# Optimization experiments

Measured on AMD Instinct MI355X. Metric: run time of the kernel, lower is better.

## Reference

```python
import jax, jax.numpy as jnp
import numpy as np

B, T, H, IN = 1024, 512, 128, 1


def setup_inputs() -> dict:
    key = jax.random.key(0)
    ks = jax.random.split(key, 12)
    s = 1.0 / np.sqrt(H)  # torch LSTMCell/Linear uniform init scale
    u = lambda k, shape: jax.random.uniform(k, shape, jnp.float32, -s, s)
    return {
        "x": jax.random.normal(ks[0], (B, T, IN), jnp.float32),
        "Wih1": u(ks[1], (4 * H, IN)),
        "Whh1": u(ks[2], (4 * H, H)),
        "bih1": u(ks[3], (4 * H,)),
        "bhh1": u(ks[4], (4 * H,)),
        "Wih2": u(ks[5], (4 * H, H)),
        "Whh2": u(ks[6], (4 * H, H)),
        "bih2": u(ks[7], (4 * H,)),
        "bhh2": u(ks[8], (4 * H,)),
        "Wl": u(ks[9], (1, H)),
        "bl": u(ks[10], (1,)),
    }


def _lstm_cell(x, h, c, Wih, Whh, bih, bhh):
    # gates: [B, 4H], torch gate order: i, f, g, o
    gates = x @ Wih.T + h @ Whh.T + (bih + bhh)
    i, f, g, o = jnp.split(gates, 4, axis=-1)
    i = jax.nn.sigmoid(i)
    f = jax.nn.sigmoid(f)
    g = jnp.tanh(g)
    o = jax.nn.sigmoid(o)
    c_new = f * c + i * g
    h_new = o * jnp.tanh(c_new)
    return h_new, c_new


def reference(x, Wih1, Whh1, bih1, bhh1, Wih2, Whh2, bih2, bhh2, Wl, bl):
    b, t, _ = x.shape
    h = Wih1.shape[0] // 4
    z = jnp.zeros((b, h), x.dtype)

    def step(carry, x_t):
        h1, c1, h2, c2 = carry
        h1, c1 = _lstm_cell(x_t, h1, c1, Wih1, Whh1, bih1, bhh1)
        h2, c2 = _lstm_cell(h1, h2, c2, Wih2, Whh2, bih2, bhh2)
        return (h1, c1, h2, c2), None

    xs = jnp.transpose(x, (1, 0, 2))  # [T, B, IN]
    (h1, c1, h2, c2), _ = jax.lax.scan(step, (z, z, z, z), xs)
    # module stacks per-step linear outputs then keeps [:, -1] -> last step only
    return h2 @ Wl.T + bl  # [B, 1]
```

## Files before the change

### kernel.cpp

```cpp
#include <hip/hip_runtime.h>
#include <hip/hip_fp16.h>

#define TT 512
#define RR 4

using f16   = _Float16;
using f16x8 = __attribute__((ext_vector_type(8))) _Float16;
using f32x4 = __attribute__((ext_vector_type(4))) float;

__device__ __forceinline__ float sigm(float x) {
    return __builtin_amdgcn_rcpf(1.0f + __builtin_amdgcn_exp2f(x * -1.44269504f));
}
__device__ __forceinline__ float tanh_(float x) {
    return 1.0f - 2.0f * __builtin_amdgcn_rcpf(1.0f + __builtin_amdgcn_exp2f(x * 2.88539008f));
}

__global__ __launch_bounds__(512, 2) void lstm2_fused(
    const float* __restrict__ x,
    const float* __restrict__ Wih1,
    const float* __restrict__ Whh1,
    const float* __restrict__ bih1,
    const float* __restrict__ bhh1,
    const float* __restrict__ Wih2,
    const float* __restrict__ Whh2,
    const float* __restrict__ bih2,
    const float* __restrict__ bhh2,
    const float* __restrict__ Wl,
    const float* __restrict__ bl,
    float* __restrict__ out)
{
    __shared__ char smem[24576];

    const int tid  = threadIdx.x;
    const int w    = tid >> 6;
    const int lane = tid & 63;
    const int r    = lane & 15;
    const int q    = lane >> 4;
    const int rowbase = blockIdx.x * RR;

    {
        unsigned* hz = (unsigned*)smem;
        #pragma unroll
        for (int i = 0; i < 8; ++i) hz[tid + i * 512] = 0u;
    }

    float b1o[4], b2o[4], w1o[4];
    #pragma unroll
    for (int g = 0; g < 4; ++g) {
        int n = g * 128 + w * 16 + r;
        b1o[g] = bih1[n] + bhh1[n];
        b2o[g] = bih2[n] + bhh2[n];
        w1o[g] = Wih1[n];
    }
    const float wlv = Wl[w * 16 + r];
    const float bl0 = bl[0];

    f16x8 wr1[4][4], w2i[4][4], w2h[4][4];
    #pragma unroll
    for (int g = 0; g < 4; ++g) {
        int n = g * 128 + w * 16 + r;
        #pragma unroll
        for (int kt = 0; kt < 4; ++kt) {
            int k0 = kt * 32 + q * 8;
            const float4* p1 = (const float4*)(Whh1 + n * 128 + k0);
            const float4* pi = (const float4*)(Wih2 + n * 128 + k0);
            const float4* ph = (const float4*)(Whh2 + n * 128 + k0);
            float4 a1v = p1[0], b1v = p1[1];
            float4 ai = pi[0], bi = pi[1];
            float4 ah = ph[0], bh = ph[1];
            wr1[g][kt] = f16x8{ (f16)a1v.x,(f16)a1v.y,(f16)a1v.z,(f16)a1v.w,
                                (f16)b1v.x,(f16)b1v.y,(f16)b1v.z,(f16)b1v.w };
            w2i[g][kt] = f16x8{ (f16)ai.x,(f16)ai.y,(f16)ai.z,(f16)ai.w,
                                (f16)bi.x,(f16)bi.y,(f16)bi.z,(f16)bi.w };
            w2h[g][kt] = f16x8{ (f16)ah.x,(f16)ah.y,(f16)ah.z,(f16)ah.w,
                                (f16)bh.x,(f16)bh.y,(f16)bh.z,(f16)bh.w };
        }
    }

    int afrag[4];
    #pragma unroll
    for (int kt = 0; kt < 4; ++kt)
        afrag[kt] = r * 256 + ((kt * 64 + q * 16) ^ ((r & 7) << 4));
    const int hwoff = q * 256 + ((w * 32 + r * 2) ^ (q << 4));
    char* const gbase = smem + 16384 + w * 1024;

    float c1 = 0.f, c2 = 0.f, h2fin = 0.f;

    __syncthreads();

    char* const h1base = smem;
    char* const h2base = smem + 8192;

    for (int t = 0; t < TT; ++t) {
        const int p = t & 1;
        char* h1r = h1base + p * 4096;
        char* h1w = h1base + (p ^ 1) * 4096;
        char* h2r = h2base + p * 4096;
        char* h2w = h2base + (p ^ 1) * 4096;

        const float xv = x[(rowbase + q) * TT + t];

        f32x4 acc[4] = {{0.f,0.f,0.f,0.f},{0.f,0.f,0.f,0.f},
                        {0.f,0.f,0.f,0.f},{0.f,0.f,0.f,0.f}};
        #pragma unroll
        for (int kt = 0; kt < 4; ++kt) {
            f16x8 a1 = *(const f16x8*)(h1r + afrag[kt]);
            #pragma unroll
            for (int g = 0; g < 4; ++g)
                acc[g] = __builtin_amdgcn_mfma_f32_16x16x32_f16(a1, wr1[g][kt], acc[g], 0, 0, 0);
        }
        if (q == 0) {
            #pragma unroll
            for (int g = 0; g < 4; ++g)
                *(f32x4*)(gbase + g * 256 + r * 16) = acc[g];
        }
        {
            float pre[4];
            #pragma unroll
            for (int g = 0; g < 4; ++g)
                pre[g] = ((const float*)(gbase + g * 256 + r * 16))[q]
                         + fmaf(xv, w1o[g], b1o[g]);
            float gi = sigm (pre[0]);
            float gf = sigm (pre[1]);
            float gg = tanh_(pre[2]);
            float go = sigm (pre[3]);
            c1 = gf * c1 + gi * gg;
            float h1v = go * tanh_(c1);
            *(f16*)(h1w + hwoff) = (f16)h1v;
        }

        __syncthreads();

        f32x4 acc2[4] = {{0.f,0.f,0.f,0.f},{0.f,0.f,0.f,0.f},
                         {0.f,0.f,0.f,0.f},{0.f,0.f,0.f,0.f}};
        #pragma unroll
        for (int kt = 0; kt < 4; ++kt) {
            f16x8 ah1 = *(const f16x8*)(h1w + afrag[kt]);
            f16x8 ah2 = *(const f16x8*)(h2r + afrag[kt]);
            #pragma unroll
            for (int g = 0; g < 4; ++g)
                acc2[g] = __builtin_amdgcn_mfma_f32_16x16x32_f16(ah1, w2i[g][kt], acc2[g], 0, 0, 0);
            #pragma unroll
            for (int g = 0; g < 4; ++g)
                acc2[g] = __builtin_amdgcn_mfma_f32_16x16x32_f16(ah2, w2h[g][kt], acc2[g], 0, 0, 0);
        }
        if (q == 0) {
            #pragma unroll
            for (int g = 0; g < 4; ++g)
                *(f32x4*)(gbase + g * 256 + r * 16) = acc2[g];
        }
        {
            float pre[4];
            #pragma unroll
            for (int g = 0; g < 4; ++g)
                pre[g] = ((const float*)(gbase + g * 256 + r * 16))[q] + b2o[g];
            float gi = sigm (pre[0]);
            float gf = sigm (pre[1]);
            float gg = tanh_(pre[2]);
            float go = sigm (pre[3]);
            c2 = gf * c2 + gi * gg;
            float h2v = go * tanh_(c2);
            h2fin = h2v;
            *(f16*)(h2w + hwoff) = (f16)h2v;
        }

        __syncthreads();
    }

    float v = h2fin * wlv;
    v += __shfl_xor(v, 1);
    v += __shfl_xor(v, 2);
    v += __shfl_xor(v, 4);
    v += __shfl_xor(v, 8);
    float* red = (float*)(smem + 16384);
    if (r == 0) red[q * 8 + w] = v;
    __syncthreads();
    if (tid < RR) {
        float a = bl0;
        #pragma unroll
        for (int s = 0; s < 8; ++s) a += red[tid * 8 + s];
        out[rowbase + tid] = a;
    }
}

extern "C" void kernel_launch(void* const* d_in, const int* in_sizes, int n_in,
                              void* d_out, int out_size, void* d_ws, size_t ws_size,
                              hipStream_t stream) {
    const float* x    = (const float*)d_in[0];
    const float* Wih1 = (const float*)d_in[1];
    const float* Whh1 = (const float*)d_in[2];
    const float* bih1 = (const float*)d_in[3];
    const float* bhh1 = (const float*)d_in[4];
    const float* Wih2 = (const float*)d_in[5];
    const float* Whh2 = (const float*)d_in[6];
    const float* bih2 = (const float*)d_in[7];
    const float* bhh2 = (const float*)d_in[8];
    const float* Wl   = (const float*)d_in[9];
    const float* bl   = (const float*)d_in[10];
    float* out = (float*)d_out;

    lstm2_fused<<<dim3(256), dim3(512), 0, stream>>>(
        x, Wih1, Whh1, bih1, bhh1, Wih2, Whh2, bih2, bhh2, Wl, bl, out);
}
```

Measured before the change: 887.7 us.

## Specialize waves per LSTM layer and pipeline layer 2 one step behind

Splits the eight waves into four layer-1 waves and four layer-2 waves, with layer 2 lagging one timestep so each iteration needs a single barrier instead of two. Each wave now covers 32 hidden units, and the layer-2 recurrent weights are staged as fp16 in a large swizzled dynamic shared buffer. This is meant to cut per-step synchronization and let both layers run concurrently. In exchange, the layer-2 waves issue twice as many MFMAs, read B fragments from LDS, and the large shared allocation limits residency to one block per CU.

```diff
diff --git a/kernel.cpp b/kernel.cpp
--- a/kernel.cpp
+++ b/kernel.cpp
@@ -15,7 +15,7 @@
     return 1.0f - 2.0f * __builtin_amdgcn_rcpf(1.0f + __builtin_amdgcn_exp2f(x * 2.88539008f));
 }
 
-__global__ __launch_bounds__(512, 2) void lstm2_fused(
+__global__ __launch_bounds__(512, 2) void lstm2_spec(
     const float* __restrict__ x,
     const float* __restrict__ Wih1,
     const float* __restrict__ Whh1,
@@ -29,7 +29,11 @@
     const float* __restrict__ bl,
     float* __restrict__ out)
 {
-    __shared__ char smem[24576];
+    extern __shared__ char smem[];
+    char* const whh2L  = smem;
+    char* const h1m    = smem + 131072;
+    char* const h2m    = smem + 133120;
+    char* const strips = smem + 135168;
 
     const int tid  = threadIdx.x;
     const int w    = tid >> 6;
@@ -37,148 +41,182 @@
     const int r    = lane & 15;
     const int q    = lane >> 4;
     const int rowbase = blockIdx.x * RR;
+    const bool isL1 = (w < 4);
+    const int  jj   = isL1 ? w : (w - 4);
 
     {
-        unsigned* hz = (unsigned*)smem;
+        unsigned* z = (unsigned*)h1m;
+        z[tid] = 0u; z[tid + 512] = 0u;
+    }
+    for (int it = 0; it < 64; ++it) {
+        int pp = tid + it * 512;
+        int n  = pp >> 6;
+        int kp = pp & 63;
+        float2 v = *(const float2*)(Whh2 + n * 128 + kp * 2);
+        union { f16 h[2]; unsigned u; } cv;
+        cv.h[0] = (f16)v.x; cv.h[1] = (f16)v.y;
+        *(unsigned*)(whh2L + n * 256 + ((kp * 4) ^ ((n & 7) << 4))) = cv.u;
+    }
+
+    float bo[2][4], w1o[2][4];
+    #pragma unroll
+    for (int t2 = 0; t2 < 2; ++t2)
         #pragma unroll
-        for (int i = 0; i < 8; ++i) hz[tid + i * 512] = 0u;
-    }
-
-    float b1o[4], b2o[4], w1o[4];
-    #pragma unroll
-    for (int g = 0; g < 4; ++g) {
-        int n = g * 128 + w * 16 + r;
-        b1o[g] = bih1[n] + bhh1[n];
-        b2o[g] = bih2[n] + bhh2[n];
-        w1o[g] = Wih1[n];
-    }
-    const float wlv = Wl[w * 16 + r];
+        for (int g = 0; g < 4; ++g) {
+            int n = g * 128 + jj * 32 + t2 * 16 + r;
+            if (isL1) { bo[t2][g] = bih1[n] + bhh1[n]; w1o[t2][g] = Wih1[n]; }
+            else      { bo[t2][g] = bih2[n] + bhh2[n]; w1o[t2][g] = 0.f; }
+        }
+    float wl0 = 0.f, wl1 = 0.f;
+    if (!isL1) { wl0 = Wl[jj * 32 + r]; wl1 = Wl[jj * 32 + 16 + r]; }
     const float bl0 = bl[0];
 
-    f16x8 wr1[4][4], w2i[4][4], w2h[4][4];
-    #pragma unroll
-    for (int g = 0; g < 4; ++g) {
-        int n = g * 128 + w * 16 + r;
+    const float* const Wreg = isL1 ? Whh1 : Wih2;
+    f16x8 wreg[4][2][4];
+    #pragma unroll
+    for (int g = 0; g < 4; ++g)
         #pragma unroll
-        for (int kt = 0; kt < 4; ++kt) {
-            int k0 = kt * 32 + q * 8;
-            const float4* p1 = (const float4*)(Whh1 + n * 128 + k0);
-            const float4* pi = (const float4*)(Wih2 + n * 128 + k0);
-            const float4* ph = (const float4*)(Whh2 + n * 128 + k0);
-            float4 a1v = p1[0], b1v = p1[1];
-            float4 ai = pi[0], bi = pi[1];
-            float4 ah = ph[0], bh = ph[1];
-            wr1[g][kt] = f16x8{ (f16)a1v.x,(f16)a1v.y,(f16)a1v.z,(f16)a1v.w,
-                                (f16)b1v.x,(f16)b1v.y,(f16)b1v.z,(f16)b1v.w };
-            w2i[g][kt] = f16x8{ (f16)ai.x,(f16)ai.y,(f16)ai.z,(f16)ai.w,
-                                (f16)bi.x,(f16)bi.y,(f16)bi.z,(f16)bi.w };
-            w2h[g][kt] = f16x8{ (f16)ah.x,(f16)ah.y,(f16)ah.z,(f16)ah.w,
-                                (f16)bh.x,(f16)bh.y,(f16)bh.z,(f16)bh.w };
+        for (int t2 = 0; t2 < 2; ++t2) {
+            int n = g * 128 + jj * 32 + t2 * 16 + r;
+            #pragma unroll
+            for (int kt = 0; kt < 4; ++kt) {
+                const float4* p = (const float4*)(Wreg + n * 128 + kt * 32 + q * 8);
+                float4 a = p[0], b = p[1];
+                wreg[g][t2][kt] = f16x8{ (f16)a.x,(f16)a.y,(f16)a.z,(f16)a.w,
+                                         (f16)b.x,(f16)b.y,(f16)b.z,(f16)b.w };
+            }
         }
-    }
-
-    int afrag[4];
-    #pragma unroll
-    for (int kt = 0; kt < 4; ++kt)
-        afrag[kt] = r * 256 + ((kt * 64 + q * 16) ^ ((r & 7) << 4));
-    const int hwoff = q * 256 + ((w * 32 + r * 2) ^ (q << 4));
-    char* const gbase = smem + 16384 + w * 1024;
-
-    float c1 = 0.f, c2 = 0.f, h2fin = 0.f;
+
+    const int swz = (r & 7) << 4;
+    int kxo[4];
+    #pragma unroll
+    for (int kt = 0; kt < 4; ++kt) kxo[kt] = (kt * 64 + q * 16) ^ swz;
+    int afo[4];
+    #pragma unroll
+    for (int kt = 0; kt < 4; ++kt) afo[kt] = r * 256 + kxo[kt];
+    int nbt[2];
+    #pragma unroll
+    for (int t2 = 0; t2 < 2; ++t2) nbt[t2] = (jj * 32 + t2 * 16 + r) * 256;
+    int hwo[2];
+    #pragma unroll
+    for (int t2 = 0; t2 < 2; ++t2) {
+        int u = jj * 32 + t2 * 16 + r;
+        hwo[t2] = q * 256 + ((2 * u) ^ (q << 4));
+    }
+    char* const strip = strips + w * 2048;
+    const bool rlow = (r < 4);
+    const f16x8 zf = f16x8{0,0,0,0,0,0,0,0};
+
+    float cst[2] = {0.f, 0.f};
+    float h2f[2] = {0.f, 0.f};
 
     __syncthreads();
 
-    char* const h1base = smem;
-    char* const h2base = smem + 8192;
-
-    for (int t = 0; t < TT; ++t) {
-        const int p = t & 1;
-        char* h1r = h1base + p * 4096;
-        char* h1w = h1base + (p ^ 1) * 4096;
-        char* h2r = h2base + p * 4096;
-        char* h2w = h2base + (p ^ 1) * 4096;
-
-        const float xv = x[(rowbase + q) * TT + t];
-
-        f32x4 acc[4] = {{0.f,0.f,0.f,0.f},{0.f,0.f,0.f,0.f},
-                        {0.f,0.f,0.f,0.f},{0.f,0.f,0.f,0.f}};
-        #pragma unroll
-        for (int kt = 0; kt < 4; ++kt) {
-            f16x8 a1 = *(const f16x8*)(h1r + afrag[kt]);
-            #pragma unroll
-            for (int g = 0; g < 4; ++g)
-                acc[g] = __builtin_amdgcn_mfma_f32_16x16x32_f16(a1, wr1[g][kt], acc[g], 0, 0, 0);
+    for (int i = 0; i <= TT; ++i) {
+        f32x4 acc[4][2] = {{{0,0,0,0},{0,0,0,0}},{{0,0,0,0},{0,0,0,0}},
+                           {{0,0,0,0},{0,0,0,0}},{{0,0,0,0},{0,0,0,0}}};
+        if (isL1) {
+            if (i < TT) {
+                const char* h1r = h1m + ((i + 1) & 1) * 1024;
+                char*       h1w = h1m + (i & 1) * 1024;
+                const float xv = x[(rowbase + q) * TT + i];
+                #pragma unroll
+                for (int kt = 0; kt < 4; ++kt) {
+                    f16x8 af = rlow ? *(const f16x8*)(h1r + afo[kt]) : zf;
+                    #pragma unroll
+                    for (int g = 0; g < 4; ++g)
+                        #pragma unroll
+                        for (int t2 = 0; t2 < 2; ++t2)
+                            acc[g][t2] = __builtin_amdgcn_mfma_f32_16x16x32_f16(
+                                af, wreg[g][t2][kt], acc[g][t2], 0, 0, 0);
+                }
+                if (q == 0) {
+                    #pragma unroll
+                    for (int g = 0; g < 4; ++g)
+                        #pragma unroll
+                        for (int t2 = 0; t2 < 2; ++t2)
+                            *(f32x4*)(strip + (g * 2 + t2) * 256 + r * 16) = acc[g][t2];
+                }
+                #pragma unroll
+                for (int t2 = 0; t2 < 2; ++t2) {
+                    float pg[4];
+                    #pragma unroll
+                    for (int g = 0; g < 4; ++g)
+                        pg[g] = ((const float*)(strip + (g * 2 + t2) * 256 + r * 16))[q]
+                                + fmaf(xv, w1o[t2][g], bo[t2][g]);
+                    float gi = sigm(pg[0]), gf = sigm(pg[1]);
+                    float gg = tanh_(pg[2]), go = sigm(pg[3]);
+                    cst[t2] = gf * cst[t2] + gi * gg;
+                    float hv = go * tanh_(cst[t2]);
+                    *(f16*)(h1w + hwo[t2]) = (f16)hv;
+                }
+            }
+        } else {
+            if (i >= 1) {
+                const char* h1r = h1m + ((i + 1) & 1) * 1024;
+                const char* h2r = h2m + (i & 1) * 1024;
+                char*       h2w = h2m + ((i + 1) & 1) * 1024;
+                #pragma unroll
+                for (int kt = 0; kt < 4; ++kt) {
+                    f16x8 af = rlow ? *(const f16x8*)(h1r + afo[kt]) : zf;
+                    #pragma unroll
+                    for (int g = 0; g < 4; ++g)
+                        #pragma unroll
+                        for (int t2 = 0; t2 < 2; ++t2)
+                            acc[g][t2] = __builtin_amdgcn_mfma_f32_16x16x32_f16(
+                                af, wreg[g][t2][kt], acc[g][t2], 0, 0, 0);
+                }
+                #pragma unroll
+                for (int kt = 0; kt < 4; ++kt) {
+                    f16x8 ah = rlow ? *(const f16x8*)(h2r + afo[kt]) : zf;
+                    #pragma unroll
+                    for (int g = 0; g < 4; ++g)
+                        #pragma unroll
+                        for (int t2 = 0; t2 < 2; ++t2) {
+                            f16x8 bf = *(const f16x8*)(whh2L + g * 32768 + nbt[t2] + kxo[kt]);
+                            acc[g][t2] = __builtin_amdgcn_mfma_f32_16x16x32_f16(
+                                ah, bf, acc[g][t2], 0, 0, 0);
+                        }
+                }
+                if (q == 0) {
+                    #pragma unroll
+                    for (int g = 0; g < 4; ++g)
+                        #pragma unroll
+                        for (int t2 = 0; t2 < 2; ++t2)
+                            *(f32x4*)(strip + (g * 2 + t2) * 256 + r * 16) = acc[g][t2];
+                }
+                #pragma unroll
+                for (int t2 = 0; t2 < 2; ++t2) {
+                    float pg[4];
+                    #pragma unroll
+                    for (int g = 0; g < 4; ++g)
+                        pg[g] = ((const float*)(strip + (g * 2 + t2) * 256 + r * 16))[q]
+                                + bo[t2][g];
+                    float gi = sigm(pg[0]), gf = sigm(pg[1]);
+                    float gg = tanh_(pg[2]), go = sigm(pg[3]);
+                    cst[t2] = gf * cst[t2] + gi * gg;
+                    float hv = go * tanh_(cst[t2]);
+                    h2f[t2] = hv;
+                    *(f16*)(h2w + hwo[t2]) = (f16)hv;
+                }
+            }
         }
-        if (q == 0) {
-            #pragma unroll
-            for (int g = 0; g < 4; ++g)
-                *(f32x4*)(gbase + g * 256 + r * 16) = acc[g];
-        }
-        {
-            float pre[4];
-            #pragma unroll
-            for (int g = 0; g < 4; ++g)
-                pre[g] = ((const float*)(gbase + g * 256 + r * 16))[q]
-                         + fmaf(xv, w1o[g], b1o[g]);
-            float gi = sigm (pre[0]);
-            float gf = sigm (pre[1]);
-            float gg = tanh_(pre[2]);
-            float go = sigm (pre[3]);
-            c1 = gf * c1 + gi * gg;
-            float h1v = go * tanh_(c1);
-            *(f16*)(h1w + hwoff) = (f16)h1v;
-        }
-
         __syncthreads();
-
-        f32x4 acc2[4] = {{0.f,0.f,0.f,0.f},{0.f,0.f,0.f,0.f},
-                         {0.f,0.f,0.f,0.f},{0.f,0.f,0.f,0.f}};
-        #pragma unroll
-        for (int kt = 0; kt < 4; ++kt) {
-            f16x8 ah1 = *(const f16x8*)(h1w + afrag[kt]);
-            f16x8 ah2 = *(const f16x8*)(h2r + afrag[kt]);
-            #pragma unroll
-            for (int g = 0; g < 4; ++g)
-                acc2[g] = __builtin_amdgcn_mfma_f32_16x16x32_f16(ah1, w2i[g][kt], acc2[g], 0, 0, 0);
-            #pragma unroll
-            for (int g = 0; g < 4; ++g)
-                acc2[g] = __builtin_amdgcn_mfma_f32_16x16x32_f16(ah2, w2h[g][kt], acc2[g], 0, 0, 0);
-        }
-        if (q == 0) {
-            #pragma unroll
-            for (int g = 0; g < 4; ++g)
-                *(f32x4*)(gbase + g * 256 + r * 16) = acc2[g];
-        }
-        {
-            float pre[4];
-            #pragma unroll
-            for (int g = 0; g < 4; ++g)
-                pre[g] = ((const float*)(gbase + g * 256 + r * 16))[q] + b2o[g];
-            float gi = sigm (pre[0]);
-            float gf = sigm (pre[1]);
-            float gg = tanh_(pre[2]);
-            float go = sigm (pre[3]);
-            c2 = gf * c2 + gi * gg;
-            float h2v = go * tanh_(c2);
-            h2fin = h2v;
-            *(f16*)(h2w + hwoff) = (f16)h2v;
-        }
-
-        __syncthreads();
-    }
-
-    float v = h2fin * wlv;
-    v += __shfl_xor(v, 1);
-    v += __shfl_xor(v, 2);
-    v += __shfl_xor(v, 4);
-    v += __shfl_xor(v, 8);
-    float* red = (float*)(smem + 16384);
-    if (r == 0) red[q * 8 + w] = v;
+    }
+
+    if (!isL1) {
+        float v = h2f[0] * wl0 + h2f[1] * wl1;
+        v += __shfl_xor(v, 1);
+        v += __shfl_xor(v, 2);
+        v += __shfl_xor(v, 4);
+        v += __shfl_xor(v, 8);
+        if (r == 0) ((float*)strips)[q * 4 + jj] = v;
+    }
     __syncthreads();
     if (tid < RR) {
         float a = bl0;
         #pragma unroll
-        for (int s = 0; s < 8; ++s) a += red[tid * 8 + s];
+        for (int s = 0; s < 4; ++s) a += ((const float*)strips)[tid * 4 + s];
         out[rowbase + tid] = a;
     }
 }
@@ -199,6 +237,10 @@
     const float* bl   = (const float*)d_in[10];
     float* out = (float*)d_out;
 
-    lstm2_fused<<<dim3(256), dim3(512), 0, stream>>>(
+    static constexpr size_t SMEM = 151552;
+    hipFuncSetAttribute(reinterpret_cast<const void*>(&lstm2_spec),
+                        hipFuncAttributeMaxDynamicSharedMemorySize, (int)SMEM);
+
+    lstm2_spec<<<dim3(256), dim3(512), SMEM, stream>>>(
         x, Wih1, Whh1, bih1, bhh1, Wih2, Whh2, bih2, bhh2, Wl, bl, out);
 }
```

Result: slower. 1.074 ms (+21.0%).

## Skew LSTM layers across timesteps to halve barriers and move Whh2 to LDS

Applied to the files above, without the earlier changes.

Restructures the time loop so layer 1 at step i and layer 2 at step i-1 are computed in the same iteration, sharing one h1 fragment load and needing only one __syncthreads per step instead of two. Whh2 weights are moved out of registers into a 128KB LDS table, which frees VGPRs but adds LDS reads inside the MFMA loop. h state buffers are compacted to the 4 real rows, with zeroed fragments for padding lanes and paired f16 stores via shuffle. The 150KB dynamic LDS footprint may cut occupancy from the two blocks per CU requested in launch bounds.

```diff
diff --git a/kernel.cpp b/kernel.cpp
--- a/kernel.cpp
+++ b/kernel.cpp
@@ -14,8 +14,13 @@
 __device__ __forceinline__ float tanh_(float x) {
     return 1.0f - 2.0f * __builtin_amdgcn_rcpf(1.0f + __builtin_amdgcn_exp2f(x * 2.88539008f));
 }
-
-__global__ __launch_bounds__(512, 2) void lstm2_fused(
+__device__ __forceinline__ f16x8 cvt8(const float* p) {
+    float4 a = ((const float4*)p)[0], b = ((const float4*)p)[1];
+    return f16x8{(f16)a.x,(f16)a.y,(f16)a.z,(f16)a.w,
+                 (f16)b.x,(f16)b.y,(f16)b.z,(f16)b.w};
+}
+
+__global__ __launch_bounds__(512, 2) void lstm2_pipe(
     const float* __restrict__ x,
     const float* __restrict__ Wih1,
     const float* __restrict__ Whh1,
@@ -29,7 +34,11 @@
     const float* __restrict__ bl,
     float* __restrict__ out)
 {
-    __shared__ char smem[24576];
+    extern __shared__ char smem[];
+    char* const w2hL   = smem;
+    char* const h1m    = smem + 131072;
+    char* const h2m    = smem + 133120;
+    char* const strips = smem + 135168;
 
     const int tid  = threadIdx.x;
     const int w    = tid >> 6;
@@ -38,10 +47,13 @@
     const int q    = lane >> 4;
     const int rowbase = blockIdx.x * RR;
 
-    {
-        unsigned* hz = (unsigned*)smem;
-        #pragma unroll
-        for (int i = 0; i < 8; ++i) hz[tid + i * 512] = 0u;
+    *(float2*)(smem + 131072 + tid * 8) = float2{0.f, 0.f};
+
+    for (int it = 0; it < 16; ++it) {
+        int pp = tid + it * 512;
+        int kp = pp >> 9;
+        int n  = pp & 511;
+        *(f16x8*)(w2hL + (kp * 512 + n) * 16) = cvt8(Whh2 + n * 128 + kp * 8);
     }
 
     float b1o[4], b2o[4], w1o[4];
@@ -55,113 +67,123 @@
     const float wlv = Wl[w * 16 + r];
     const float bl0 = bl[0];
 
-    f16x8 wr1[4][4], w2i[4][4], w2h[4][4];
+    f16x8 wr1[4][4], w2i[4][4];
     #pragma unroll
     for (int g = 0; g < 4; ++g) {
         int n = g * 128 + w * 16 + r;
         #pragma unroll
         for (int kt = 0; kt < 4; ++kt) {
             int k0 = kt * 32 + q * 8;
-            const float4* p1 = (const float4*)(Whh1 + n * 128 + k0);
-            const float4* pi = (const float4*)(Wih2 + n * 128 + k0);
-            const float4* ph = (const float4*)(Whh2 + n * 128 + k0);
-            float4 a1v = p1[0], b1v = p1[1];
-            float4 ai = pi[0], bi = pi[1];
-            float4 ah = ph[0], bh = ph[1];
-            wr1[g][kt] = f16x8{ (f16)a1v.x,(f16)a1v.y,(f16)a1v.z,(f16)a1v.w,
-                                (f16)b1v.x,(f16)b1v.y,(f16)b1v.z,(f16)b1v.w };
-            w2i[g][kt] = f16x8{ (f16)ai.x,(f16)ai.y,(f16)ai.z,(f16)ai.w,
-                                (f16)bi.x,(f16)bi.y,(f16)bi.z,(f16)bi.w };
-            w2h[g][kt] = f16x8{ (f16)ah.x,(f16)ah.y,(f16)ah.z,(f16)ah.w,
-                                (f16)bh.x,(f16)bh.y,(f16)bh.z,(f16)bh.w };
-        }
-    }
-
-    int afrag[4];
+            wr1[g][kt] = cvt8(Whh1 + n * 128 + k0);
+            w2i[g][kt] = cvt8(Wih2 + n * 128 + k0);
+        }
+    }
+
+    int afm[4];
     #pragma unroll
     for (int kt = 0; kt < 4; ++kt)
-        afrag[kt] = r * 256 + ((kt * 64 + q * 16) ^ ((r & 7) << 4));
-    const int hwoff = q * 256 + ((w * 32 + r * 2) ^ (q << 4));
-    char* const gbase = smem + 16384 + w * 1024;
+        afm[kt] = (r & 3) * 256 + ((kt * 64 + q * 16) ^ ((r & 3) << 5));
+    const bool rlow = (r < 4);
+    const f16x8 zf = f16x8{0,0,0,0,0,0,0,0};
+    const int hwb = q * 256 + (((w << 5) + 2 * r) ^ (q << 5));
+    char* const strip = strips + w * 2048;
 
     float c1 = 0.f, c2 = 0.f, h2fin = 0.f;
 
     __syncthreads();
 
-    char* const h1base = smem;
-    char* const h2base = smem + 8192;
-
-    for (int t = 0; t < TT; ++t) {
-        const int p = t & 1;
-        char* h1r = h1base + p * 4096;
-        char* h1w = h1base + (p ^ 1) * 4096;
-        char* h2r = h2base + p * 4096;
-        char* h2w = h2base + (p ^ 1) * 4096;
-
-        const float xv = x[(rowbase + q) * TT + t];
-
-        f32x4 acc[4] = {{0.f,0.f,0.f,0.f},{0.f,0.f,0.f,0.f},
-                        {0.f,0.f,0.f,0.f},{0.f,0.f,0.f,0.f}};
+    for (int i = 0; i <= TT; ++i) {
+        const int p = i & 1, pp = p ^ 1;
+        const bool doL1 = (i < TT), doL2 = (i > 0);
+
+        f16x8 a1[4], ah2[4];
         #pragma unroll
         for (int kt = 0; kt < 4; ++kt) {
-            f16x8 a1 = *(const f16x8*)(h1r + afrag[kt]);
+            f16x8 v = *(const f16x8*)(h1m + pp * 1024 + afm[kt]);
+            a1[kt] = rlow ? v : zf;
+        }
+        if (doL2) {
+            #pragma unroll
+            for (int kt = 0; kt < 4; ++kt) {
+                f16x8 v = *(const f16x8*)(h2m + p * 1024 + afm[kt]);
+                ah2[kt] = rlow ? v : zf;
+            }
+        }
+        const float xv = doL1 ? x[(rowbase + q) * TT + i] : 0.f;
+
+        f32x4 acc1[4] = {{0,0,0,0},{0,0,0,0},{0,0,0,0},{0,0,0,0}};
+        f32x4 acc2[4] = {{0,0,0,0},{0,0,0,0},{0,0,0,0},{0,0,0,0}};
+        if (doL1) {
             #pragma unroll
             for (int g = 0; g < 4; ++g)
-                acc[g] = __builtin_amdgcn_mfma_f32_16x16x32_f16(a1, wr1[g][kt], acc[g], 0, 0, 0);
-        }
+                #pragma unroll
+                for (int kt = 0; kt < 4; ++kt)
+                    acc1[g] = __builtin_amdgcn_mfma_f32_16x16x32_f16(
+                        a1[kt], wr1[g][kt], acc1[g], 0, 0, 0);
+        }
+        if (doL2) {
+            #pragma unroll
+            for (int g = 0; g < 4; ++g) {
+                #pragma unroll
+                for (int kt = 0; kt < 4; ++kt)
+                    acc2[g] = __builtin_amdgcn_mfma_f32_16x16x32_f16(
+                        a1[kt], w2i[g][kt], acc2[g], 0, 0, 0);
+                #pragma unroll
+                for (int kt = 0; kt < 4; ++kt) {
+                    f16x8 bf = *(const f16x8*)(w2hL +
+                        ((kt * 4 + q) * 512 + g * 128 + w * 16 + r) * 16);
+                    acc2[g] = __builtin_amdgcn_mfma_f32_16x16x32_f16(
+                        ah2[kt], bf, acc2[g], 0, 0, 0);
+                }
+            }
+        }
+
         if (q == 0) {
+            if (doL1) {
+                #pragma unroll
+                for (int g = 0; g < 4; ++g)
+                    *(f32x4*)(strip + g * 256 + r * 16) = acc1[g];
+            }
+            if (doL2) {
+                #pragma unroll
+                for (int g = 0; g < 4; ++g)
+                    *(f32x4*)(strip + 1024 + g * 256 + r * 16) = acc2[g];
+            }
+        }
+
+        if (doL1) {
+            float pg[4];
             #pragma unroll
             for (int g = 0; g < 4; ++g)
-                *(f32x4*)(gbase + g * 256 + r * 16) = acc[g];
-        }
-        {
-            float pre[4];
+                pg[g] = ((const float*)(strip + g * 256 + r * 16))[q]
+                        + fmaf(xv, w1o[g], b1o[g]);
+            float gi = sigm(pg[0]), gf = sigm(pg[1]);
+            float gg = tanh_(pg[2]), go = sigm(pg[3]);
+            c1 = gf * c1 + gi * gg;
+            float hv = go * tanh_(c1);
+            float hn = __shfl_xor(hv, 1);
+            if ((r & 1) == 0) {
+                union { f16 h[2]; unsigned u; } pk;
+                pk.h[0] = (f16)hv; pk.h[1] = (f16)hn;
+                *(unsigned*)(h1m + p * 1024 + hwb) = pk.u;
+            }
+        }
+        if (doL2) {
+            float pg[4];
             #pragma unroll
             for (int g = 0; g < 4; ++g)
-                pre[g] = ((const float*)(gbase + g * 256 + r * 16))[q]
-                         + fmaf(xv, w1o[g], b1o[g]);
-            float gi = sigm (pre[0]);
-            float gf = sigm (pre[1]);
-            float gg = tanh_(pre[2]);
-            float go = sigm (pre[3]);
-            c1 = gf * c1 + gi * gg;
-            float h1v = go * tanh_(c1);
-            *(f16*)(h1w + hwoff) = (f16)h1v;
-        }
-
-        __syncthreads();
-
-        f32x4 acc2[4] = {{0.f,0.f,0.f,0.f},{0.f,0.f,0.f,0.f},
-                         {0.f,0.f,0.f,0.f},{0.f,0.f,0.f,0.f}};
-        #pragma unroll
-        for (int kt = 0; kt < 4; ++kt) {
-            f16x8 ah1 = *(const f16x8*)(h1w + afrag[kt]);
-            f16x8 ah2 = *(const f16x8*)(h2r + afrag[kt]);
-            #pragma unroll
-            for (int g = 0; g < 4; ++g)
-                acc2[g] = __builtin_amdgcn_mfma_f32_16x16x32_f16(ah1, w2i[g][kt], acc2[g], 0, 0, 0);
-            #pragma unroll
-            for (int g = 0; g < 4; ++g)
-                acc2[g] = __builtin_amdgcn_mfma_f32_16x16x32_f16(ah2, w2h[g][kt], acc2[g], 0, 0, 0);
-        }
-        if (q == 0) {
-            #pragma unroll
-            for (int g = 0; g < 4; ++g)
-                *(f32x4*)(gbase + g * 256 + r * 16) = acc2[g];
-        }
-        {
-            float pre[4];
-            #pragma unroll
-            for (int g = 0; g < 4; ++g)
-                pre[g] = ((const float*)(gbase + g * 256 + r * 16))[q] + b2o[g];
-            float gi = sigm (pre[0]);
-            float gf = sigm (pre[1]);
-            float gg = tanh_(pre[2]);
-            float go = sigm (pre[3]);
+                pg[g] = ((const float*)(strip + 1024 + g * 256 + r * 16))[q] + b2o[g];
+            float gi = sigm(pg[0]), gf = sigm(pg[1]);
+            float gg = tanh_(pg[2]), go = sigm(pg[3]);
             c2 = gf * c2 + gi * gg;
-            float h2v = go * tanh_(c2);
-            h2fin = h2v;
-            *(f16*)(h2w + hwoff) = (f16)h2v;
+            float hv = go * tanh_(c2);
+            h2fin = hv;
+            float hn = __shfl_xor(hv, 1);
+            if ((r & 1) == 0) {
+                union { f16 h[2]; unsigned u; } pk;
+                pk.h[0] = (f16)hv; pk.h[1] = (f16)hn;
+                *(unsigned*)(h2m + pp * 1024 + hwb) = pk.u;
+            }
         }
 
         __syncthreads();
@@ -172,7 +194,7 @@
     v += __shfl_xor(v, 2);
     v += __shfl_xor(v, 4);
     v += __shfl_xor(v, 8);
-    float* red = (float*)(smem + 16384);
+    float* red = (float*)strips;
     if (r == 0) red[q * 8 + w] = v;
     __syncthreads();
     if (tid < RR) {
@@ -199,6 +221,10 @@
     const float* bl   = (const float*)d_in[10];
     float* out = (float*)d_out;
 
-    lstm2_fused<<<dim3(256), dim3(512), 0, stream>>>(
+    static constexpr size_t SMEM = 151552;
+    hipFuncSetAttribute(reinterpret_cast<const void*>(&lstm2_pipe),
+                        hipFuncAttributeMaxDynamicSharedMemorySize, (int)SMEM);
+
+    lstm2_pipe<<<dim3(256), dim3(512), SMEM, stream>>>(
         x, Wih1, Whh1, bih1, bhh1, Wih2, Whh2, bih2, bhh2, Wl, bl, out);
 }
```

New measurement: 1.013 ms. +14.1%, slower.
